# Performance work log

Measured on AMD Instinct MI355X. Metric: run time of the kernel, lower is better.

## Reference

```python
import jax, jax.numpy as jnp
import numpy as np

K = 3  # kernel_size
P = 1  # padding (must satisfy K == 2*P+1 for the original einsum to be shape-valid)


def setup_inputs() -> dict:
    key = jax.random.key(0)
    k1, k2, k3 = jax.random.split(key, 3)
    b, i, c, L, o = 16, 64, 4, 4096, 64
    x = jax.random.normal(k1, (b, i, c, L), dtype=jnp.float32)
    time_tensor = jax.random.uniform(k2, (b, c, L), dtype=jnp.float32)
    weights = jax.random.normal(k3, (o, i, c, K), dtype=jnp.float32)
    return {"x": x, "time_tensor": time_tensor, "weights": weights}


def reference(x, time_tensor, weights):
    """x: (b,i,c,L), time_tensor: (b,c,L), weights: (o,i,c,K) -> (b,o,c,L).

    Faithful to the torch module: pad x/time by P on the time axis, unfold x
    into sliding windows, pad the unfolded tensor again by P, multiply by the
    time scalar per (b,c,l) and contract over (i,k), then crop P from each end.
    The time factor is scalar per output element, so we factor it out of the
    einsum instead of materializing the (b,o,i,c,k,l) dynamic_weights tensor --
    mathematically identical, massively cheaper.
    """
    xp = jnp.pad(x, ((0, 0), (0, 0), (0, 0), (P, P)))            # (b,i,c,L+2P)
    tp = jnp.pad(time_tensor, ((0, 0), (0, 0), (P, P)))          # (b,c,L+2P)
    Lw = xp.shape[-1] - K + 1                                    # == L since K=2P+1
    # unfold -> (b,i,c,K,Lw), matching torch's permute(0,2,1,4,3) after transpose
    xu = jnp.stack([xp[..., j:j + Lw] for j in range(K)], axis=-2)
    xu = jnp.transpose(xu, (0, 2, 1, 3, 4))                      # (b,c,i,K,Lw)
    xu = jnp.pad(xu, ((0, 0), (0, 0), (0, 0), (0, 0), (P, P)))   # (b,c,i,K,Lw+2P)
    conv = jnp.einsum('oick,bcikl->bocl', weights, xu)           # (b,o,c,L+2P)
    out = conv * tp[:, None, :, :]
    return out[..., P:-P]                                        # (b,o,c,L)
```

## Files before the change

kernel.cpp:

```cpp
#include <hip/hip_runtime.h>


#define NB 16
#define NI 64
#define NC 4
#define NL 4096
#define NO 64
#define KW 3
#define LT 64
#define NT 4
#define LBLK (LT * NT)
#define ROWS (LBLK + 2)
#define ROWB 128

#define W_PACK_BYTES (NO * NI * NC * KW * 2)

typedef float f32x4 __attribute__((ext_vector_type(4)));
typedef short bf16x8 __attribute__((ext_vector_type(8)));
typedef unsigned int u32x2 __attribute__((ext_vector_type(2)));

__device__ inline unsigned short f2bf(float f) {
    unsigned int u = __builtin_bit_cast(unsigned int, f);
    u += 0x7FFFu + ((u >> 16) & 1u);
    return (unsigned short)(u >> 16);
}

__global__ __launch_bounds__(256)
void prepack_w_kernel(const float* __restrict__ w, unsigned short* __restrict__ wp) {
    const int idx = blockIdx.x * 256 + threadIdx.x;
    const float v = w[idx];
    const int k = idx % 3;
    int r = idx / 3;
    const int c = r & 3;  r >>= 2;
    const int i = r & 63;
    const int o = r >> 6;
    const int cc   = k * 2 + (i >> 5);
    const int lane = (((i >> 3) & 3) << 4) | (o & 15);
    const int j    = i & 7;
    const int wv   = o >> 4;
    wp[(((c * 4 + wv) * 6 + cc) * 64 + lane) * 8 + j] = f2bf(v);
}

__device__ __forceinline__ void stage_load(const float* __restrict__ xb,
                                           int l0, int g, f32x4 s[4]) {
    const float* p = xb + (size_t)(4 * g) * (NC * NL) + l0;
    s[0] = *(const f32x4*)(p);
    s[1] = *(const f32x4*)(p + NC * NL);
    s[2] = *(const f32x4*)(p + 2 * NC * NL);
    s[3] = *(const f32x4*)(p + 3 * NC * NL);
}

__device__ __forceinline__ void stage_write(char* __restrict__ lds,
                                            int r0, int g, const f32x4 s[4]) {
#pragma unroll
    for (int r = 0; r < 4; ++r) {
        const int rr = r0 + r;
        u32x2 pk;
        pk[0] = (unsigned int)f2bf(s[0][r]) | ((unsigned int)f2bf(s[1][r]) << 16);
        pk[1] = (unsigned int)f2bf(s[2][r]) | ((unsigned int)f2bf(s[3][r]) << 16);
        *(u32x2*)(lds + rr * ROWB + ((8 * g) ^ ((rr & 7) << 4))) = pk;
    }
}

__device__ __forceinline__ void compute_store(const char* __restrict__ lds,
                                              const bf16x8 wfrag[6],
                                              const float* __restrict__ tb,
                                              float* __restrict__ ob,
                                              int t, int lb0, int lane) {
    const int lcol  = lane & 15;
    const int ksub2 = (lane >> 4) * 16;
    const int lbt   = lb0 + t * LT;

    f32x4 tv[4];
#pragma unroll
    for (int lt = 0; lt < 4; ++lt)
        tv[lt] = *(const f32x4*)(tb + lbt + lt * 16 + (lane >> 4) * 4);

    f32x4 acc[4] = {};
#pragma unroll
    for (int lt = 0; lt < 4; ++lt) {
#pragma unroll
        for (int cc = 0; cc < 6; ++cc) {
            const int k    = cc >> 1;
            const int ih   = cc & 1;
            const int row  = t * LT + lt * 16 + lcol + k;
            const int colb = ih * 64 + ksub2;
            const int off  = row * ROWB + (colb ^ ((row & 7) << 4));
            const bf16x8 xf = *(const bf16x8*)(lds + off);
            acc[lt] = __builtin_amdgcn_mfma_f32_16x16x32_bf16(xf, wfrag[cc], acc[lt], 0, 0, 0);
        }
    }
#pragma unroll
    for (int lt = 0; lt < 4; ++lt) {
        const int l0 = lbt + lt * 16 + (lane >> 4) * 4;
        f32x4 r;
#pragma unroll
        for (int q = 0; q < 4; ++q) r[q] = acc[lt][q] * tv[lt][q];
        *(f32x4*)(ob + l0) = r;
    }
}

__global__ __launch_bounds__(256, 4)
void tconv_mfma_kernel(const float* __restrict__ x,
                       const float* __restrict__ tt,
                       const unsigned short* __restrict__ wp,
                       float* __restrict__ out)
{
    __shared__ char lds[ROWS * ROWB];

    const int t    = threadIdx.x;
    const int lane = t & 63;
    const int wave = t >> 6;
    const int c    = blockIdx.y;
    const int b    = blockIdx.z;
    const int lb0  = blockIdx.x * LBLK;
    const int o0   = wave * 16;
    const int quad = lane & 15;
    const int g    = wave * 4 + (lane >> 4);
    const int lq   = 4 * quad;

    bf16x8 wfrag[6];
    {
        const bf16x8* wpb = (const bf16x8*)wp + (size_t)((c * 4 + wave) * 6) * 64 + lane;
#pragma unroll
        for (int cc = 0; cc < 6; ++cc) wfrag[cc] = wpb[cc * 64];
    }

    const float* xb = x + ((size_t)b * NI * NC + c) * NL;
    const float* tb = tt + (size_t)(b * NC + c) * NL;
    float* ob = out + ((size_t)b * NO * NC + (size_t)(o0 + (lane & 15)) * NC + c) * NL;

    f32x4 s0[4], s1[4];
    stage_load(xb, lb0 + 0 * LT + lq, g, s0);
    stage_load(xb, lb0 + 1 * LT + lq, g, s1);
    float h = 0.f; int hrow = 0, hcol = 0;
    if (t < 128) {
        const int which = t & 1;
        const int i     = t >> 1;
        hrow = which ? (LBLK + 1) : 0;
        hcol = 2 * i;
        const int lh = which ? (lb0 + LBLK) : (lb0 - 1);
        if (lh >= 0 && lh < NL) h = xb[(size_t)i * (NC * NL) + lh];
    }
    stage_write(lds, 1 + 0 * LT + lq, g, s0);
    stage_write(lds, 1 + 1 * LT + lq, g, s1);
    if (t < 128)
        *(unsigned short*)(lds + hrow * ROWB + (hcol ^ ((hrow & 7) << 4))) = f2bf(h);
    __syncthreads();

    stage_load(xb, lb0 + 2 * LT + lq, g, s0);
    compute_store(lds, wfrag, tb, ob, 0, lb0, lane);
    stage_write(lds, 1 + 2 * LT + lq, g, s0);
    __syncthreads();

    stage_load(xb, lb0 + 3 * LT + lq, g, s1);
    compute_store(lds, wfrag, tb, ob, 1, lb0, lane);
    stage_write(lds, 1 + 3 * LT + lq, g, s1);
    __syncthreads();

    compute_store(lds, wfrag, tb, ob, 2, lb0, lane);
    compute_store(lds, wfrag, tb, ob, 3, lb0, lane);
}

extern "C" void kernel_launch(void* const* d_in, const int* in_sizes, int n_in,
                              void* d_out, int out_size, void* d_ws, size_t ws_size,
                              hipStream_t stream) {
    const float* x  = (const float*)d_in[0];
    const float* tt = (const float*)d_in[1];
    const float* w  = (const float*)d_in[2];
    float* out = (float*)d_out;
    unsigned short* wpck = (unsigned short*)d_ws;

    dim3 block(256);
    prepack_w_kernel<<<dim3(NO * NI * NC * KW / 256), block, 0, stream>>>(w, wpck);

    dim3 grid(NL / LBLK, NC, NB);
    tconv_mfma_kernel<<<grid, block, 0, stream>>>(x, tt, wpck, out);
}
```

Before: 33.60 us.

## Fuse weight prepack into conv kernel, stage time tensor in LDS, prefetch earlier

Drops the separate weight-prepack launch. Each wave now gathers its fp32 weight fragments straight from global memory and converts them to bf16 in registers. The time-tensor slice is loaded once per block into LDS rather than read from global in every compute step. The last x stage is also loaded earlier so more loads are in flight. This removes one kernel launch and its workspace round-trip, at the cost of redundant strided weight gathers in every block and higher register pressure from the extra prefetch.

```diff
diff --git a/kernel.cpp b/kernel.cpp
--- a/kernel.cpp
+++ b/kernel.cpp
@@ -12,8 +12,8 @@
 #define LBLK (LT * NT)
 #define ROWS (LBLK + 2)
 #define ROWB 128
-
-#define W_PACK_BYTES (NO * NI * NC * KW * 2)
+#define TOFF (ROWS * ROWB)
+#define LDSB (TOFF + LBLK * 4)
 
 typedef float f32x4 __attribute__((ext_vector_type(4)));
 typedef short bf16x8 __attribute__((ext_vector_type(8)));
@@ -23,22 +23,6 @@
     unsigned int u = __builtin_bit_cast(unsigned int, f);
     u += 0x7FFFu + ((u >> 16) & 1u);
     return (unsigned short)(u >> 16);
-}
-
-__global__ __launch_bounds__(256)
-void prepack_w_kernel(const float* __restrict__ w, unsigned short* __restrict__ wp) {
-    const int idx = blockIdx.x * 256 + threadIdx.x;
-    const float v = w[idx];
-    const int k = idx % 3;
-    int r = idx / 3;
-    const int c = r & 3;  r >>= 2;
-    const int i = r & 63;
-    const int o = r >> 6;
-    const int cc   = k * 2 + (i >> 5);
-    const int lane = (((i >> 3) & 3) << 4) | (o & 15);
-    const int j    = i & 7;
-    const int wv   = o >> 4;
-    wp[(((c * 4 + wv) * 6 + cc) * 64 + lane) * 8 + j] = f2bf(v);
 }
 
 __device__ __forceinline__ void stage_load(const float* __restrict__ xb,
@@ -64,17 +48,15 @@
 
 __device__ __forceinline__ void compute_store(const char* __restrict__ lds,
                                               const bf16x8 wfrag[6],
-                                              const float* __restrict__ tb,
                                               float* __restrict__ ob,
                                               int t, int lb0, int lane) {
     const int lcol  = lane & 15;
     const int ksub2 = (lane >> 4) * 16;
-    const int lbt   = lb0 + t * LT;
 
     f32x4 tv[4];
 #pragma unroll
     for (int lt = 0; lt < 4; ++lt)
-        tv[lt] = *(const f32x4*)(tb + lbt + lt * 16 + (lane >> 4) * 4);
+        tv[lt] = *(const f32x4*)(lds + TOFF + 4 * (t * LT + lt * 16 + (lane >> 4) * 4));
 
     f32x4 acc[4] = {};
 #pragma unroll
@@ -92,7 +74,7 @@
     }
 #pragma unroll
     for (int lt = 0; lt < 4; ++lt) {
-        const int l0 = lbt + lt * 16 + (lane >> 4) * 4;
+        const int l0 = lb0 + t * LT + lt * 16 + (lane >> 4) * 4;
         f32x4 r;
 #pragma unroll
         for (int q = 0; q < 4; ++q) r[q] = acc[lt][q] * tv[lt][q];
@@ -103,10 +85,10 @@
 __global__ __launch_bounds__(256, 4)
 void tconv_mfma_kernel(const float* __restrict__ x,
                        const float* __restrict__ tt,
-                       const unsigned short* __restrict__ wp,
+                       const float* __restrict__ w,
                        float* __restrict__ out)
 {
-    __shared__ char lds[ROWS * ROWB];
+    __shared__ char lds[LDSB];
 
     const int t    = threadIdx.x;
     const int lane = t & 63;
@@ -115,16 +97,8 @@
     const int b    = blockIdx.z;
     const int lb0  = blockIdx.x * LBLK;
     const int o0   = wave * 16;
-    const int quad = lane & 15;
     const int g    = wave * 4 + (lane >> 4);
-    const int lq   = 4 * quad;
-
-    bf16x8 wfrag[6];
-    {
-        const bf16x8* wpb = (const bf16x8*)wp + (size_t)((c * 4 + wave) * 6) * 64 + lane;
-#pragma unroll
-        for (int cc = 0; cc < 6; ++cc) wfrag[cc] = wpb[cc * 64];
-    }
+    const int lq   = 4 * (lane & 15);
 
     const float* xb = x + ((size_t)b * NI * NC + c) * NL;
     const float* tb = tt + (size_t)(b * NC + c) * NL;
@@ -142,24 +116,52 @@
         const int lh = which ? (lb0 + LBLK) : (lb0 - 1);
         if (lh >= 0 && lh < NL) h = xb[(size_t)i * (NC * NL) + lh];
     }
+    const float tval = tb[lb0 + t];
+
+    bf16x8 wfrag[6];
+    {
+        const float* wl = w + (size_t)(o0 + (lane & 15)) * (NI * NC * KW)
+                            + (size_t)((lane >> 4) * 8) * (NC * KW) + c * KW;
+#pragma unroll
+        for (int half = 0; half < 2; ++half) {
+            float v[3][8];
+#pragma unroll
+            for (int cc3 = 0; cc3 < 3; ++cc3) {
+                const int cc = half * 3 + cc3;
+                const float* p = wl + (cc & 1) * (32 * NC * KW) + (cc >> 1);
+#pragma unroll
+                for (int j = 0; j < 8; ++j) v[cc3][j] = p[j * (NC * KW)];
+            }
+#pragma unroll
+            for (int cc3 = 0; cc3 < 3; ++cc3) {
+                bf16x8 a;
+#pragma unroll
+                for (int j = 0; j < 8; ++j) a[j] = (short)f2bf(v[cc3][j]);
+                wfrag[half * 3 + cc3] = a;
+            }
+        }
+    }
+
     stage_write(lds, 1 + 0 * LT + lq, g, s0);
     stage_write(lds, 1 + 1 * LT + lq, g, s1);
     if (t < 128)
         *(unsigned short*)(lds + hrow * ROWB + (hcol ^ ((hrow & 7) << 4))) = f2bf(h);
+    *(float*)(lds + TOFF + 4 * t) = tval;
     __syncthreads();
 
     stage_load(xb, lb0 + 2 * LT + lq, g, s0);
-    compute_store(lds, wfrag, tb, ob, 0, lb0, lane);
+    stage_load(xb, lb0 + 3 * LT + lq, g, s1);
+
+    compute_store(lds, wfrag, ob, 0, lb0, lane);
     stage_write(lds, 1 + 2 * LT + lq, g, s0);
     __syncthreads();
 
-    stage_load(xb, lb0 + 3 * LT + lq, g, s1);
-    compute_store(lds, wfrag, tb, ob, 1, lb0, lane);
+    compute_store(lds, wfrag, ob, 1, lb0, lane);
     stage_write(lds, 1 + 3 * LT + lq, g, s1);
     __syncthreads();
 
-    compute_store(lds, wfrag, tb, ob, 2, lb0, lane);
-    compute_store(lds, wfrag, tb, ob, 3, lb0, lane);
+    compute_store(lds, wfrag, ob, 2, lb0, lane);
+    compute_store(lds, wfrag, ob, 3, lb0, lane);
 }
 
 extern "C" void kernel_launch(void* const* d_in, const int* in_sizes, int n_in,
@@ -169,11 +171,8 @@
     const float* tt = (const float*)d_in[1];
     const float* w  = (const float*)d_in[2];
     float* out = (float*)d_out;
-    unsigned short* wpck = (unsigned short*)d_ws;
 
     dim3 block(256);
-    prepack_w_kernel<<<dim3(NO * NI * NC * KW / 256), block, 0, stream>>>(w, wpck);
-
     dim3 grid(NL / LBLK, NC, NB);
-    tconv_mfma_kernel<<<grid, block, 0, stream>>>(x, tt, wpck, out);
+    tconv_mfma_kernel<<<grid, block, 0, stream>>>(x, tt, w, out);
 }
```

Result: no change. 33.81 us (+0.6%).

## Stage time tensor in LDS, issue loads earlier, use lightweight LDS barriers

Applied to the files above, without the earlier changes.

Loads the block's time-tensor slice once into LDS instead of having each wave reload it from global memory. The third x stage load is issued before the first compute, and the weight-fragment loads are moved after the x/halo loads, so more global traffic is in flight early. __syncthreads is replaced with a barrier that waits only on LDS counters, so outstanding global loads need not drain at each barrier. The cost is extra LDS space and more live registers for two staging buffers, which could lower occupancy.

```diff
diff --git a/kernel.cpp b/kernel.cpp
--- a/kernel.cpp
+++ b/kernel.cpp
@@ -12,6 +12,8 @@
 #define LBLK (LT * NT)
 #define ROWS (LBLK + 2)
 #define ROWB 128
+#define TOFF (ROWS * ROWB)
+#define LDSB (TOFF + LBLK * 4)
 
 #define W_PACK_BYTES (NO * NI * NC * KW * 2)
 
@@ -23,6 +25,12 @@
     unsigned int u = __builtin_bit_cast(unsigned int, f);
     u += 0x7FFFu + ((u >> 16) & 1u);
     return (unsigned short)(u >> 16);
+}
+
+__device__ __forceinline__ void block_sync_lds() {
+    asm volatile("s_waitcnt lgkmcnt(0)" ::: "memory");
+    __builtin_amdgcn_s_barrier();
+    asm volatile("" ::: "memory");
 }
 
 __global__ __launch_bounds__(256)
@@ -64,17 +72,15 @@
 
 __device__ __forceinline__ void compute_store(const char* __restrict__ lds,
                                               const bf16x8 wfrag[6],
-                                              const float* __restrict__ tb,
                                               float* __restrict__ ob,
                                               int t, int lb0, int lane) {
     const int lcol  = lane & 15;
     const int ksub2 = (lane >> 4) * 16;
-    const int lbt   = lb0 + t * LT;
 
     f32x4 tv[4];
 #pragma unroll
     for (int lt = 0; lt < 4; ++lt)
-        tv[lt] = *(const f32x4*)(tb + lbt + lt * 16 + (lane >> 4) * 4);
+        tv[lt] = *(const f32x4*)(lds + TOFF + 4 * (t * LT + lt * 16 + (lane >> 4) * 4));
 
     f32x4 acc[4] = {};
 #pragma unroll
@@ -92,7 +98,7 @@
     }
 #pragma unroll
     for (int lt = 0; lt < 4; ++lt) {
-        const int l0 = lbt + lt * 16 + (lane >> 4) * 4;
+        const int l0 = lb0 + t * LT + lt * 16 + (lane >> 4) * 4;
         f32x4 r;
 #pragma unroll
         for (int q = 0; q < 4; ++q) r[q] = acc[lt][q] * tv[lt][q];
@@ -106,7 +112,7 @@
                        const unsigned short* __restrict__ wp,
                        float* __restrict__ out)
 {
-    __shared__ char lds[ROWS * ROWB];
+    __shared__ char lds[LDSB];
 
     const int t    = threadIdx.x;
     const int lane = t & 63;
@@ -115,16 +121,8 @@
     const int b    = blockIdx.z;
     const int lb0  = blockIdx.x * LBLK;
     const int o0   = wave * 16;
-    const int quad = lane & 15;
     const int g    = wave * 4 + (lane >> 4);
-    const int lq   = 4 * quad;
-
-    bf16x8 wfrag[6];
-    {
-        const bf16x8* wpb = (const bf16x8*)wp + (size_t)((c * 4 + wave) * 6) * 64 + lane;
-#pragma unroll
-        for (int cc = 0; cc < 6; ++cc) wfrag[cc] = wpb[cc * 64];
-    }
+    const int lq   = 4 * (lane & 15);
 
     const float* xb = x + ((size_t)b * NI * NC + c) * NL;
     const float* tb = tt + (size_t)(b * NC + c) * NL;
@@ -142,24 +140,35 @@
         const int lh = which ? (lb0 + LBLK) : (lb0 - 1);
         if (lh >= 0 && lh < NL) h = xb[(size_t)i * (NC * NL) + lh];
     }
+    const float tval = tb[lb0 + t];
+
+    bf16x8 wfrag[6];
+    {
+        const bf16x8* wpb = (const bf16x8*)wp + (size_t)((c * 4 + wave) * 6) * 64 + lane;
+#pragma unroll
+        for (int cc = 0; cc < 6; ++cc) wfrag[cc] = wpb[cc * 64];
+    }
+
     stage_write(lds, 1 + 0 * LT + lq, g, s0);
     stage_write(lds, 1 + 1 * LT + lq, g, s1);
     if (t < 128)
         *(unsigned short*)(lds + hrow * ROWB + (hcol ^ ((hrow & 7) << 4))) = f2bf(h);
-    __syncthreads();
+    *(float*)(lds + TOFF + 4 * t) = tval;
+    block_sync_lds();
 
     stage_load(xb, lb0 + 2 * LT + lq, g, s0);
-    compute_store(lds, wfrag, tb, ob, 0, lb0, lane);
+    stage_load(xb, lb0 + 3 * LT + lq, g, s1);
+
+    compute_store(lds, wfrag, ob, 0, lb0, lane);
     stage_write(lds, 1 + 2 * LT + lq, g, s0);
-    __syncthreads();
+    block_sync_lds();
 
-    stage_load(xb, lb0 + 3 * LT + lq, g, s1);
-    compute_store(lds, wfrag, tb, ob, 1, lb0, lane);
+    compute_store(lds, wfrag, ob, 1, lb0, lane);
     stage_write(lds, 1 + 3 * LT + lq, g, s1);
-    __syncthreads();
+    block_sync_lds();
 
-    compute_store(lds, wfrag, tb, ob, 2, lb0, lane);
-    compute_store(lds, wfrag, tb, ob, 3, lb0, lane);
+    compute_store(lds, wfrag, ob, 2, lb0, lane);
+    compute_store(lds, wfrag, ob, 3, lb0, lane);
 }
 
 extern "C" void kernel_launch(void* const* d_in, const int* in_sizes, int n_in,
```

Result: no change. 33.48 us (-0.4%).
